# Optimization experiments

Hardware: AMD Instinct MI355X
Metric: run time of the kernel (lower is better)

## Reference

```python
import jax, jax.numpy as jnp
import numpy as np

B, S, D, H = 2, 2048, 2048, 16
HD = D // H
FF = 4 * D
EPS = 1e-5
SCALE = 1.0 / np.sqrt(D)  # source uses 1/sqrt(d_out), not 1/sqrt(head_dim)


def _gelu_tanh(x):
    c = np.sqrt(2.0 / np.pi).astype(np.float32)
    return 0.5 * x * (1.0 + jnp.tanh(c * (x + 0.044715 * x * x * x)))


def _layernorm(x, scale, shift):
    mean = jnp.mean(x, axis=-1, keepdims=True)
    var = jnp.mean(jnp.square(x - mean), axis=-1, keepdims=True)  # correction=0
    return (x - mean) * jax.lax.rsqrt(var + EPS) * scale + shift


def setup_inputs() -> dict:
    key = jax.random.key(0)
    ks = jax.random.split(key, 10)
    init = lambda k, shape, fan_in: (jax.random.normal(k, shape, jnp.float32) / np.sqrt(fan_in))
    return {
        "x": jax.random.normal(ks[0], (B, S, D), jnp.float32),
        "wq": init(ks[1], (D, D), D),
        "wk": init(ks[2], (D, D), D),
        "wv": init(ks[3], (D, D), D),
        "wo": init(ks[4], (D, D), D),
        "bo": jnp.zeros((D,), jnp.float32),
        "g1": jnp.ones((D,), jnp.float32),
        "s1": jnp.zeros((D,), jnp.float32),
        "g2": jnp.ones((D,), jnp.float32),
        "s2": jnp.zeros((D,), jnp.float32),
        "w1": init(ks[5], (D, FF), D),
        "b1": jnp.zeros((FF,), jnp.float32),
        "w2": init(ks[6], (FF, D), FF),
        "b2": jnp.zeros((D,), jnp.float32),
    }


def _block(x, wq, wk, wv, wo, bo, g1, s1, g2, s2, w1, b1, w2, b2):
    # pre-LN attention
    h = _layernorm(x, g1, s1)
    q = (h @ wq).reshape(B, S, H, HD).transpose(0, 2, 1, 3)  # [B,H,S,HD]
    k = (h @ wk).reshape(B, S, H, HD).transpose(0, 2, 1, 3)
    v = (h @ wv).reshape(B, S, H, HD).transpose(0, 2, 1, 3)
    scores = jnp.einsum('bhqd,bhkd->bhqk', q, k) * SCALE
    causal = jnp.tril(jnp.ones((S, S), dtype=bool))  # mask strictly-upper
    scores = jnp.where(causal, scores, -jnp.inf)
    attn = jax.nn.softmax(scores, axis=-1)
    ctx = jnp.einsum('bhqk,bhkd->bhqd', attn, v)
    ctx = ctx.transpose(0, 2, 1, 3).reshape(B, S, D)
    x = x + ctx @ wo + bo
    # pre-LN FFN
    h = _layernorm(x, g2, s2)
    h = _gelu_tanh(h @ w1 + b1) @ w2 + b2
    return x + h


def reference(x, wq, wk, wv, wo, bo, g1, s1, g2, s2, w1, b1, w2, b2):
    return _block(x, wq, wk, wv, wo, bo, g1, s1, g2, s2, w1, b1, w2, b2)
```

## Files before the change

kernel.cpp:

```cpp
#include <hip/hip_runtime.h>
#include <hip/hip_bf16.h>
#include <cstdint>

constexpr float SCALE_QK = 0.02209708691207961f;
constexpr float LOG2E    = 1.4426950408889634f;

using short8 = __attribute__((ext_vector_type(8))) short;
using f32x4  = __attribute__((ext_vector_type(4))) float;
using ushort4v = __attribute__((ext_vector_type(4))) ushort;

#define MFMA16(a,b,c) __builtin_amdgcn_mfma_f32_16x16x32_bf16((a),(b),(c),0,0,0)

__device__ __forceinline__ ushort f2bf(float f){
  uint32_t u = __builtin_bit_cast(uint32_t, f);
  u += 0x7fffu + ((u >> 16) & 1u);
  return (ushort)(u >> 16);
}

__device__ __forceinline__ void gload_lds16(const void* g, void* l){
  __builtin_amdgcn_global_load_lds(
      (const __attribute__((address_space(1))) void*)g,
      (__attribute__((address_space(3))) void*)l, 16, 0, 0);
}

#define VMCNT(n) asm volatile("s_waitcnt vmcnt(" #n ")" ::: "memory")
#define SBAR() do{ __builtin_amdgcn_s_barrier(); \
  asm volatile("" ::: "memory"); }while(0)

__global__ __launch_bounds__(256) void ln_kernel(
    const float* __restrict__ x, const float* __restrict__ g,
    const float* __restrict__ sh, ushort* __restrict__ out){
  const int row = blockIdx.x, t = threadIdx.x;
  const float* xr = x + (size_t)row*2048 + t*8;
  float v[8];
  *(float4*)&v[0] = *(const float4*)(xr);
  *(float4*)&v[4] = *(const float4*)(xr + 4);
  float s = 0.f, sq = 0.f;
#pragma unroll
  for (int i = 0; i < 8; ++i){ s += v[i]; sq += v[i]*v[i]; }
#pragma unroll
  for (int d = 1; d < 64; d <<= 1){ s += __shfl_xor(s, d, 64); sq += __shfl_xor(sq, d, 64); }
  __shared__ float red[8];
  const int w = t >> 6, lane = t & 63;
  if (lane == 0){ red[w] = s; red[4 + w] = sq; }
  __syncthreads();
  s  = red[0] + red[1] + red[2] + red[3];
  sq = red[4] + red[5] + red[6] + red[7];
  const float mean = s * (1.f/2048.f);
  const float inv  = rsqrtf(sq * (1.f/2048.f) - mean*mean + 1e-5f);
  union { ushort u[8]; uint4 v4; } o;
#pragma unroll
  for (int i = 0; i < 8; ++i){
    int j = t*8 + i;
    o.u[i] = f2bf((v[i] - mean) * inv * g[j] + sh[j]);
  }
  *(uint4*)(out + (size_t)row*2048 + t*8) = o.v4;
}

__global__ __launch_bounds__(256) void wconv_t(
    const float* __restrict__ in, ushort* __restrict__ out, int K, int N){
  __shared__ ushort tile[32][34];
  const int tx = threadIdx.x & 31, ty = threadIdx.x >> 5;
  const int n0 = blockIdx.x * 32, k0 = blockIdx.y * 32;
#pragma unroll
  for (int r = 0; r < 4; ++r){
    int kk = ty + r*8;
    tile[kk][tx] = f2bf(in[(size_t)(k0 + kk)*N + n0 + tx]);
  }
  __syncthreads();
#pragma unroll
  for (int r = 0; r < 4; ++r){
    int nn = ty + r*8;
    out[(size_t)(n0 + nn)*K + k0 + tx] = tile[tx][nn];
  }
}

__global__ __launch_bounds__(256) void wconv4(
    const float* __restrict__ w0, const float* __restrict__ w1p,
    const float* __restrict__ w2p, const float* __restrict__ w3p,
    ushort* __restrict__ out){
  __shared__ ushort tile[32][34];
  const int tx = threadIdx.x & 31, ty = threadIdx.x >> 5;
  const int n0 = blockIdx.x * 32, k0 = blockIdx.y * 32, z = blockIdx.z;
  const float* in = (z == 0) ? w0 : (z == 1) ? w1p : (z == 2) ? w2p : w3p;
  ushort* o = out + (size_t)z * 4194304;
#pragma unroll
  for (int r = 0; r < 4; ++r){
    int kk = ty + r*8;
    tile[kk][tx] = f2bf(in[(size_t)(k0 + kk)*2048 + n0 + tx]);
  }
  __syncthreads();
#pragma unroll
  for (int r = 0; r < 4; ++r){
    int nn = ty + r*8;
    o[(size_t)(n0 + nn)*2048 + k0 + tx] = tile[tx][nn];
  }
}

#define MM(qd) do{ __builtin_amdgcn_s_setprio(1); \
  _Pragma("unroll") for (int mi = 0; mi < 4; ++mi) \
  _Pragma("unroll") for (int ni = 0; ni < 2; ++ni) \
  _Pragma("unroll") for (int kk = 0; kk < 2; ++kk) \
    acc[qd][mi][ni] = MFMA16(af[mi][kk], bf[ni][kk], acc[qd][mi][ni]); \
  __builtin_amdgcn_s_setprio(0); }while(0)

template<int EPI>
__global__ __launch_bounds__(512, 2) void gemm8p(
    const ushort* __restrict__ A, const ushort* __restrict__ Bt,
    int N, int K, void* __restrict__ outp, const float* __restrict__ bias){
  __shared__ ushort Al[2][2][128*64];
  __shared__ ushort Bl[2][2][128*64];
  const int tid = threadIdx.x, lane = tid & 63, wid = tid >> 6;
  const int l15 = lane & 15, l4 = lane >> 4;
  const int wrr = wid >> 2, wcc = wid & 3;

  const int bid = blockIdx.x;
  const int xcd = bid & 7, jj = bid >> 3;
  const int m0 = (xcd*2 + (jj & 1)) * 256;
  const int n0 = (jj >> 1) * 256;

  const ushort* Abase = A  + (size_t)m0*K;
  const ushort* Bbase = Bt + (size_t)n0*K;

  f32x4 acc[4][4][2];
#pragma unroll
  for (int q = 0; q < 4; ++q)
#pragma unroll
    for (int mi = 0; mi < 4; ++mi)
#pragma unroll
      for (int ni = 0; ni < 2; ++ni) acc[q][mi][ni] = (f32x4){0.f,0.f,0.f,0.f};

  auto stageA = [&](int buf, int h, int kt){
#pragma unroll
    for (int l = 0; l < 2; ++l){
      const int c = l*512 + tid, r = c >> 3, s = (c & 7) ^ ((c >> 3) & 7);
      gload_lds16(Abase + (size_t)(h*128 + r)*K + (size_t)kt*64 + s*8,
                  &Al[buf][h][c*8]);
    }
  };
  auto stageB = [&](int buf, int h, int kt){
#pragma unroll
    for (int l = 0; l < 2; ++l){
      const int c = l*512 + tid, r = c >> 3, s = (c & 7) ^ ((c >> 3) & 7);
      gload_lds16(Bbase + (size_t)(h*128 + r)*K + (size_t)kt*64 + s*8,
                  &Bl[buf][h][c*8]);
    }
  };

  short8 af[4][2], bf[2][2];
  auto readA = [&](int buf, int h){
#pragma unroll
    for (int mi = 0; mi < 4; ++mi){
      const int r = wrr*64 + mi*16 + l15;
#pragma unroll
      for (int kk = 0; kk < 2; ++kk)
        af[mi][kk] = *(const short8*)&Al[buf][h][r*64 + (((kk*4 + l4) ^ (r & 7))*8)];
    }
  };
  auto readB = [&](int buf, int h){
#pragma unroll
    for (int ni = 0; ni < 2; ++ni){
      const int r = wcc*32 + ni*16 + l15;
#pragma unroll
      for (int kk = 0; kk < 2; ++kk)
        bf[ni][kk] = *(const short8*)&Bl[buf][h][r*64 + (((kk*4 + l4) ^ (r & 7))*8)];
    }
  };

  const int NT = K >> 6;
  stageA(0,0,0); stageB(0,0,0); stageB(0,1,0); stageA(0,1,0);
  VMCNT(4); SBAR();

  for (int kt = 0; kt < NT - 1; ++kt){
    const int cur = kt & 1, nxt = cur ^ 1;
    readA(cur,0); readB(cur,0);
    stageA(nxt,0,kt+1);
    VMCNT(4); SBAR();
    MM(0); SBAR();
    readB(cur,1);
    stageB(nxt,0,kt+1);
    VMCNT(4); SBAR();
    MM(1); SBAR();
    readA(cur,1);
    stageB(nxt,1,kt+1);
    SBAR();
    MM(2); SBAR();
    readB(cur,0);
    stageA(nxt,1,kt+1);
    VMCNT(4); SBAR();
    MM(3); SBAR();
  }
  {
    const int cur = (NT - 1) & 1;
    readA(cur,0); readB(cur,0); VMCNT(2); SBAR(); MM(0); SBAR();
    readB(cur,1);               VMCNT(0); SBAR(); MM(1); SBAR();
    readA(cur,1);                         SBAR(); MM(2); SBAR();
    readB(cur,0);                         SBAR(); MM(3); SBAR();
  }

#pragma unroll
  for (int qd = 0; qd < 4; ++qd){
    const int qr = qd >> 1, qc = qr ^ (qd & 1);
#pragma unroll
    for (int mi = 0; mi < 4; ++mi){
#pragma unroll
      for (int ni = 0; ni < 2; ++ni){
        const int mrow = m0 + qr*128 + wrr*64 + mi*16 + l4*4;
        const int col  = n0 + qc*128 + wcc*32 + ni*16 + l15;
#pragma unroll
        for (int j2 = 0; j2 < 4; ++j2){
          const float xx = acc[qd][mi][ni][j2] + bias[col];
          const float z  = 0.7978845608f*(xx + 0.044715f*xx*xx*xx);
          const float t  = __expf(-2.f*fabsf(z));
          const float th = (1.f - t)/(1.f + t);
          const float gl = 0.5f*xx*(1.f + copysignf(th, xx));
          ((ushort*)outp)[(size_t)(mrow + j2)*N + col] = f2bf(gl);
        }
      }
    }
  }
}

template<int EPI>
__global__ __launch_bounds__(256) void gemm_bt(
    const ushort* __restrict__ A, const ushort* __restrict__ Bt,
    int N, int K, void* __restrict__ outp,
    const float* __restrict__ resid, const float* __restrict__ bias){
  __shared__ ushort lds[2][128*64];
  const int tid = threadIdx.x, lane = tid & 63, wid = tid >> 6;
  const int wr = wid >> 1, wc = wid & 1;
  const int l15 = lane & 15, l4 = lane >> 4;

  const int bid = blockIdx.x;
  const int xcd = bid & 7, j = bid >> 3;
  const int mb = xcd*4 + (j & 3);
  const int nb = j >> 2;
  const int m0 = mb * 128, n0 = nb * 128;

  f32x4 acc[4][4];
#pragma unroll
  for (int mi = 0; mi < 4; ++mi)
#pragma unroll
    for (int ni = 0; ni < 4; ++ni) acc[mi][ni] = (f32x4){0.f,0.f,0.f,0.f};

  const ushort* Abase = A  + (size_t)m0*K;
  const ushort* Bbase = Bt + (size_t)n0*K;

  const int NTk = K >> 6;
  for (int kt = 0; kt < NTk; ++kt){
    if (kt) __syncthreads();
#pragma unroll
    for (int i = 0; i < 4; ++i){
      const int chunk = (i*4 + wid)*64 + lane;
      const int row = chunk >> 3;
      const int c8  = (chunk & 7) ^ (row & 7);
      const size_t goff = (size_t)row*K + (size_t)kt*64 + c8*8;
      gload_lds16(Abase + goff, (ushort*)&lds[0][0] + (size_t)(i*4 + wid)*512);
      gload_lds16(Bbase + goff, (ushort*)&lds[1][0] + (size_t)(i*4 + wid)*512);
    }
    __syncthreads();

#pragma unroll
    for (int kk = 0; kk < 2; ++kk){
      short8 af[4], bf[4];
      const int kb = kk*4 + l4;
#pragma unroll
      for (int i = 0; i < 4; ++i){
        const int rA = wr*64 + i*16 + l15;
        af[i] = *(const short8*)&lds[0][rA*64 + ((kb ^ (rA & 7))*8)];
        const int rB = wc*64 + i*16 + l15;
        bf[i] = *(const short8*)&lds[1][rB*64 + ((kb ^ (rB & 7))*8)];
      }
#pragma unroll
      for (int mi = 0; mi < 4; ++mi)
#pragma unroll
        for (int ni = 0; ni < 4; ++ni)
          acc[mi][ni] = MFMA16(af[mi], bf[ni], acc[mi][ni]);
    }
  }

  if constexpr (EPI == 0){
    __syncthreads();
    ushort* tile = (ushort*)&lds[0][0];
    const int which = n0 >> 11;
    const int hh = (n0 & 2047) >> 7;
    const int bb = m0 >> 11, srow0 = m0 & 2047;
    if (which != 2){
      const float qs = (which == 0) ? SCALE_QK * LOG2E : 1.0f;
#pragma unroll
      for (int mi = 0; mi < 4; ++mi)
#pragma unroll
        for (int ni = 0; ni < 4; ++ni){
          const int rl = wr*64 + mi*16 + l4*4;
          const int cl = wc*64 + ni*16 + l15;
#pragma unroll
          for (int j2 = 0; j2 < 4; ++j2)
            tile[(rl + j2)*128 + cl] = f2bf(acc[mi][ni][j2] * qs);
        }
      __syncthreads();
      ushort* dst = (ushort*)outp + (size_t)which*8388608 +
                    ((size_t)(bb*16 + hh)*2048 + srow0)*128;
#pragma unroll
      for (int i = 0; i < 8; ++i){
        const int c = i*256 + tid, row = c >> 4, d8 = (c & 15)*8;
        *(uint4*)(dst + (size_t)row*128 + d8) = *(const uint4*)&tile[row*128 + d8];
      }
    } else {
#pragma unroll
      for (int mi = 0; mi < 4; ++mi)
#pragma unroll
        for (int ni = 0; ni < 4; ++ni){
          const int rl = wr*64 + mi*16 + l4*4;
          const int cl = wc*64 + ni*16 + l15;
          ushort4v o;
#pragma unroll
          for (int j2 = 0; j2 < 4; ++j2) o[j2] = f2bf(acc[mi][ni][j2]);
          *(ushort4v*)&tile[cl*128 + rl] = o;
        }
      __syncthreads();
      ushort* dst = (ushort*)outp + (size_t)2*8388608 +
                    (size_t)(bb*16 + hh)*262144 + srow0;
#pragma unroll
      for (int i = 0; i < 8; ++i){
        const int c = i*256 + tid, drow = c >> 4, s8 = (c & 15)*8;
        *(uint4*)(dst + (size_t)drow*2048 + s8) = *(const uint4*)&tile[drow*128 + s8];
      }
    }
  } else {
#pragma unroll
    for (int mi = 0; mi < 4; ++mi){
#pragma unroll
      for (int ni = 0; ni < 4; ++ni){
        const int rloc = wr*64 + mi*16 + l4*4;
        const int col  = n0 + wc*64 + ni*16 + l15;
#pragma unroll
        for (int j2 = 0; j2 < 4; ++j2){
          const int m = m0 + rloc + j2;
          float v = acc[mi][ni][j2];
          if constexpr (EPI == 1){
            ((float*)outp)[(size_t)m*N + col] = resid[(size_t)m*N + col] + bias[col] + v;
          } else {
            const float xx = v + bias[col];
            const float z  = 0.7978845608f*(xx + 0.044715f*xx*xx*xx);
            const float t  = __expf(-2.f*fabsf(z));
            const float th = (1.f - t)/(1.f + t);
            const float gl = 0.5f*xx*(1.f + copysignf(th, xx));
            ((ushort*)outp)[(size_t)m*N + col] = f2bf(gl);
          }
        }
      }
    }
  }
}

__global__ __launch_bounds__(256, 2) void attn_kernel(
    const ushort* __restrict__ q, const ushort* __restrict__ k,
    const ushort* __restrict__ vt, ushort* __restrict__ ctx){
  __shared__ ushort k_lds[2][64*128];
  __shared__ ushort v_lds[2][128*64];
  __shared__ ushort p_lds[4][32*64];
  const int tid = threadIdx.x, lane = tid & 63, w = tid >> 6;
  const int l15 = lane & 15, l4 = lane >> 4;
  const int id = blockIdx.x;
  const int bh = id & 31;
  const int r  = id >> 5;
  const int qt = (r < 8) ? (15 - r) : (r - 8);
  const int bb = bh >> 4, hh = bh & 15;
  const ushort* kbase = k  + (size_t)bh * 262144;
  const ushort* vbase = vt + (size_t)bh * 262144;

  short8 qf[2][4];
#pragma unroll
  for (int mi = 0; mi < 2; ++mi){
    const int s = qt*128 + w*32 + mi*16 + l15;
    const ushort* qr = q + ((size_t)bh*2048 + s)*128 + l4*8;
#pragma unroll
    for (int kk = 0; kk < 4; ++kk) qf[mi][kk] = *(const short8*)(qr + kk*32);
  }

  f32x4 cacc[2][8];
#pragma unroll
  for (int mi = 0; mi < 2; ++mi)
#pragma unroll
    for (int dt = 0; dt < 8; ++dt) cacc[mi][dt] = (f32x4){0.f,0.f,0.f,0.f};
  float mrun[2][4], lrun[2][4];
#pragma unroll
  for (int mi = 0; mi < 2; ++mi)
#pragma unroll
    for (int j = 0; j < 4; ++j){ mrun[mi][j] = -1e30f; lrun[mi][j] = 0.f; }

  auto stage = [&](int buf, int t){
    const ushort* ksrc = kbase + (size_t)t*8192;
#pragma unroll
    for (int i = 0; i < 4; ++i){
      const int base = i*256 + w*64;
      const int chunk = base + lane;
      const int kr = chunk >> 4;
      const int c8 = (chunk & 15) ^ (kr & 7);
      gload_lds16(ksrc + (size_t)kr*128 + c8*8, &k_lds[buf][(size_t)base*8]);
    }
#pragma unroll
    for (int i = 0; i < 4; ++i){
      const int base = i*256 + w*64;
      const int chunk = base + lane;
      const int vr = chunk >> 3;
      const int c8 = (chunk & 7) ^ (vr & 7);
      gload_lds16(vbase + (size_t)vr*2048 + t*64 + c8*8, &v_lds[buf][(size_t)base*8]);
    }
  };

  const int nt = 2*qt + 2;
  stage(0, 0);
  __syncthreads();
  int cur = 0;
  for (int t = 0; t < nt; ++t){
    if (t + 1 < nt) stage(cur ^ 1, t + 1);

    const bool skip = (t == 2*qt + 1) && (w < 2);
    if (!skip){
      f32x4 sa[2][4];
#pragma unroll
      for (int mi = 0; mi < 2; ++mi)
#pragma unroll
        for (int ct = 0; ct < 4; ++ct) sa[mi][ct] = (f32x4){0.f,0.f,0.f,0.f};
      __builtin_amdgcn_s_setprio(1);
#pragma unroll
      for (int kk = 0; kk < 4; ++kk){
#pragma unroll
        for (int ct = 0; ct < 4; ++ct){
          const int kr = ct*16 + l15;
          short8 kf = *(const short8*)&k_lds[cur][kr*128 + (((kk*4 + l4) ^ (kr & 7))*8)];
          sa[0][ct] = MFMA16(qf[0][kk], kf, sa[0][ct]);
          sa[1][ct] = MFMA16(qf[1][kk], kf, sa[1][ct]);
        }
      }
      __builtin_amdgcn_s_setprio(0);

      const bool anymask = (t >= 2*qt) && !((t == 2*qt) && (w >= 2));
      float rowmax[2][4];
      bool grow = false;
#pragma unroll
      for (int mi = 0; mi < 2; ++mi){
#pragma unroll
        for (int j = 0; j < 4; ++j){
          const int qa = qt*128 + w*32 + mi*16 + l4*4 + j;
          float mx = -1e30f;
#pragma unroll
          for (int ct = 0; ct < 4; ++ct){
            float sc = sa[mi][ct][j];
            if (anymask){
              const int ka = t*64 + ct*16 + l15;
              sc = (ka > qa) ? -1e30f : sc;
            }
            sa[mi][ct][j] = sc;
            mx = fmaxf(mx, sc);
          }
#pragma unroll
          for (int d = 1; d < 16; d <<= 1) mx = fmaxf(mx, __shfl_xor(mx, d, 16));
          rowmax[mi][j] = mx;
          grow = grow || (mx > mrun[mi][j] + 8.f);
        }
      }
      if (__any(grow)){
#pragma unroll
        for (int mi = 0; mi < 2; ++mi)
#pragma unroll
          for (int j = 0; j < 4; ++j){
            const float mnew = fmaxf(mrun[mi][j], rowmax[mi][j]);
            const float corr = exp2f(mrun[mi][j] - mnew);
            mrun[mi][j] = mnew; lrun[mi][j] *= corr;
#pragma unroll
            for (int dt = 0; dt < 8; ++dt) cacc[mi][dt][j] *= corr;
          }
      }
#pragma unroll
      for (int mi = 0; mi < 2; ++mi)
#pragma unroll
        for (int j = 0; j < 4; ++j){
          float psum = 0.f;
#pragma unroll
          for (int ct = 0; ct < 4; ++ct){
            const float p = exp2f(sa[mi][ct][j] - mrun[mi][j]);
            sa[mi][ct][j] = p; psum += p;
          }
          lrun[mi][j] += psum;
        }

#pragma unroll
      for (int mi = 0; mi < 2; ++mi)
#pragma unroll
        for (int ct = 0; ct < 4; ++ct)
#pragma unroll
          for (int j = 0; j < 4; ++j){
            const int row = mi*16 + l4*4 + j, col = ct*16 + l15;
            p_lds[w][row*64 + ((col >> 3) ^ (row & 7))*8 + (col & 7)] = f2bf(sa[mi][ct][j]);
          }

      __builtin_amdgcn_s_setprio(1);
#pragma unroll
      for (int kk2 = 0; kk2 < 2; ++kk2){
        const int kb = kk2*4 + l4;
        short8 pa0 = *(const short8*)&p_lds[w][l15*64 + ((kb ^ (l15 & 7))*8)];
        short8 pa1 = *(const short8*)&p_lds[w][(16 + l15)*64 + ((kb ^ (l15 & 7))*8)];
#pragma unroll
        for (int dt = 0; dt < 8; ++dt){
          const int vr = dt*16 + l15;
          short8 vf = *(const short8*)&v_lds[cur][vr*64 + ((kb ^ (vr & 7))*8)];
          cacc[0][dt] = MFMA16(pa0, vf, cacc[0][dt]);
          cacc[1][dt] = MFMA16(pa1, vf, cacc[1][dt]);
        }
      }
      __builtin_amdgcn_s_setprio(0);
    }

    if (t + 1 < nt){ __syncthreads(); cur ^= 1; }
  }

#pragma unroll
  for (int mi = 0; mi < 2; ++mi){
    float inv[4];
#pragma unroll
    for (int j = 0; j < 4; ++j){
      float lt = lrun[mi][j];
#pragma unroll
      for (int d = 1; d < 16; d <<= 1) lt += __shfl_xor(lt, d, 16);
      inv[j] = 1.f / lt;
    }
#pragma unroll
    for (int dt = 0; dt < 8; ++dt)
#pragma unroll
      for (int j = 0; j < 4; ++j){
        const int s = qt*128 + w*32 + mi*16 + l4*4 + j;
        const int d = dt*16 + l15;
        ctx[((size_t)(bb*2048 + s))*2048 + hh*128 + d] = f2bf(cacc[mi][dt][j] * inv[j]);
      }
  }
}

extern "C" void kernel_launch(void* const* d_in, const int* in_sizes, int n_in,
                              void* d_out, int out_size, void* d_ws, size_t ws_size,
                              hipStream_t stream) {
  const float* x  = (const float*)d_in[0];
  const float* wq = (const float*)d_in[1];
  const float* wk = (const float*)d_in[2];
  const float* wv = (const float*)d_in[3];
  const float* wo = (const float*)d_in[4];
  const float* bo = (const float*)d_in[5];
  const float* g1 = (const float*)d_in[6];
  const float* s1 = (const float*)d_in[7];
  const float* g2 = (const float*)d_in[8];
  const float* s2 = (const float*)d_in[9];
  const float* w1 = (const float*)d_in[10];
  const float* b1 = (const float*)d_in[11];
  const float* w2 = (const float*)d_in[12];
  const float* b2 = (const float*)d_in[13];
  float* out = (float*)d_out;
  char* ws = (char*)d_ws;

  ushort* wqkvT = (ushort*)(ws + 0);
  ushort* woT = (ushort*)(ws + 25165824);
  ushort* w1T = (ushort*)(ws + 33554432);
  ushort* w2T = (ushort*)(ws + 67108864);
  ushort* h1  = (ushort*)(ws + 100663296);
  ushort* qb  = (ushort*)(ws + 117440512);
  ushort* kb  = (ushort*)(ws + 134217728);
  ushort* vtb = (ushort*)(ws + 150994944);
  ushort* ctxb= (ushort*)(ws + 184549376);
  float*  x2  = (float*)(ws + 201326592);
  ushort* h2  = (ushort*)(ws + 234881024);
  ushort* ffb = (ushort*)(ws + 117440512);

  wconv4<<<dim3(64, 64, 4), 256, 0, stream>>>(wq, wk, wv, wo, wqkvT);
  wconv_t<<<dim3(256, 64), 256, 0, stream>>>(w1, w1T, 2048, 8192);
  wconv_t<<<dim3(64, 256), 256, 0, stream>>>(w2, w2T, 8192, 2048);

  ln_kernel<<<4096, 256, 0, stream>>>(x, g1, s1, h1);

  gemm_bt<0><<<32*48, 256, 0, stream>>>(h1, wqkvT, 6144, 2048, qb, nullptr, nullptr);

  attn_kernel<<<512, 256, 0, stream>>>(qb, kb, vtb, ctxb);

  gemm_bt<1><<<32*16, 256, 0, stream>>>(ctxb, woT, 2048, 2048, x2, x, bo);

  ln_kernel<<<4096, 256, 0, stream>>>(x2, g2, s2, h2);

  gemm8p<2><<<512, 512, 0, stream>>>(h2, w1T, 8192, 2048, ffb, b1);
  gemm_bt<1><<<32*16, 256, 0, stream>>>(ffb, w2T, 2048, 8192, out, x2, b2);

  (void)in_sizes; (void)n_in; (void)out_size; (void)ws_size;
}
```

Measured before the change: 708.2 us.

## Deepen FFN1 GEMM prefetch so half-tiles load two k-steps ahead

Reworks the software pipeline of the 8-wave FFN1 GEMM so that some LDS half-buffers are refilled for k-step t+2 as soon as they are consumed, rather than only staging t+1. This cuts the number of vmcnt waits per iteration to one, giving global loads more time to land behind the MFMA work. The change depends on getting the buffer reuse order and wait counts exactly right, and any mistake there would cause an LDS data race.

```diff
diff --git a/kernel.cpp b/kernel.cpp
--- a/kernel.cpp
+++ b/kernel.cpp
@@ -105,7 +105,7 @@
   __builtin_amdgcn_s_setprio(0); }while(0)
 
 template<int EPI>
-__global__ __launch_bounds__(512, 2) void gemm8p(
+__global__ __launch_bounds__(512, 2) void gemm8p2(
     const ushort* __restrict__ A, const ushort* __restrict__ Bt,
     int N, int K, void* __restrict__ outp, const float* __restrict__ bias){
   __shared__ ushort Al[2][2][128*64];
@@ -169,33 +169,28 @@
 
   const int NT = K >> 6;
   stageA(0,0,0); stageB(0,0,0); stageB(0,1,0); stageA(0,1,0);
-  VMCNT(4); SBAR();
-
-  for (int kt = 0; kt < NT - 1; ++kt){
-    const int cur = kt & 1, nxt = cur ^ 1;
+  if (NT > 1){ stageA(1,0,1); stageB(1,1,1); VMCNT(4); }
+  else        { VMCNT(0); }
+  SBAR();
+
+  for (int t = 0; t < NT; ++t){
+    const int cur = t & 1, nxt = cur ^ 1;
     readA(cur,0); readB(cur,0);
-    stageA(nxt,0,kt+1);
-    VMCNT(4); SBAR();
-    MM(0); SBAR();
+    if (t+1 < NT) stageA(nxt,1,t+1);
+    SBAR(); MM(0); SBAR();
     readB(cur,1);
-    stageB(nxt,0,kt+1);
-    VMCNT(4); SBAR();
-    MM(1); SBAR();
+    if (t+1 < NT) stageB(nxt,0,t+1);
+    SBAR(); MM(1); SBAR();
     readA(cur,1);
-    stageB(nxt,1,kt+1);
+    if (t+2 < NT) stageA(cur,0,t+2);
+    SBAR(); MM(2); SBAR();
+    readB(cur,0);
+    if (t+2 < NT) stageB(cur,1,t+2);
+    SBAR(); MM(3);
+    if (t+1 < NT){
+      if (t+2 < NT){ VMCNT(4); } else { VMCNT(0); }
+    }
     SBAR();
-    MM(2); SBAR();
-    readB(cur,0);
-    stageA(nxt,1,kt+1);
-    VMCNT(4); SBAR();
-    MM(3); SBAR();
-  }
-  {
-    const int cur = (NT - 1) & 1;
-    readA(cur,0); readB(cur,0); VMCNT(2); SBAR(); MM(0); SBAR();
-    readB(cur,1);               VMCNT(0); SBAR(); MM(1); SBAR();
-    readA(cur,1);                         SBAR(); MM(2); SBAR();
-    readB(cur,0);                         SBAR(); MM(3); SBAR();
   }
 
 #pragma unroll
@@ -584,7 +579,7 @@
 
   ln_kernel<<<4096, 256, 0, stream>>>(x2, g2, s2, h2);
 
-  gemm8p<2><<<512, 512, 0, stream>>>(h2, w1T, 8192, 2048, ffb, b1);
+  gemm8p2<2><<<512, 512, 0, stream>>>(h2, w1T, 8192, 2048, ffb, b1);
   gemm_bt<1><<<32*16, 256, 0, stream>>>(ffb, w2T, 2048, 8192, out, x2, b2);
 
   (void)in_sizes; (void)n_in; (void)out_size; (void)ws_size;
```

Result: no change. 713.6 us (+0.8%).
